# Kernel optimization log

Hardware: AMD Instinct MI355X
Metric: run time of the kernel (lower is better)

Reference implementation:

```python
import jax, jax.numpy as jnp
import numpy as np

D = 384
EPS = 1e-12  # F.normalize eps


def setup_inputs() -> dict:
    key = jax.random.key(0)
    ks = jax.random.split(key, 12)
    s = 1.0 / np.sqrt(D)  # torch Linear default init scale
    return {
        "x": jax.random.normal(ks[0], (8192, D), jnp.float32),
        "y": jax.random.normal(ks[1], (8192, D), jnp.float32),
        "Wq": jax.random.uniform(ks[2], (D, D), jnp.float32, -s, s),
        "bq": jax.random.uniform(ks[3], (D,), jnp.float32, -s, s),
        "Wk": jax.random.uniform(ks[4], (D, D), jnp.float32, -s, s),
        "bk": jax.random.uniform(ks[5], (D,), jnp.float32, -s, s),
        "Wv": jax.random.uniform(ks[6], (D, D), jnp.float32, -s, s),
        "bv": jax.random.uniform(ks[7], (D,), jnp.float32, -s, s),
        "Wo": jax.random.uniform(ks[8], (D, D), jnp.float32, -s, s),
        "bo": jax.random.uniform(ks[9], (D,), jnp.float32, -s, s),
    }


def reference(x, y, Wq, bq, Wk, bk, Wv, bv, Wo, bo):
    # Q: [N, d], K/V: [M, d]
    Q = x @ Wq.T + bq
    K = y @ Wk.T + bk
    V = y @ Wv.T + bv
    scale = 1.0 / jnp.sqrt(jnp.asarray(Q.shape[-1], Q.dtype))
    attn = jax.nn.softmax((Q @ K.T) * scale, axis=-1)  # [N, M]
    ctx = attn @ V  # [N, d]
    # F.normalize(p=2, dim=1): divide by max(||row||_2, eps)
    norm = jnp.maximum(jnp.linalg.norm(ctx, axis=1, keepdims=True), EPS)
    ctx = ctx / norm
    return (x + ctx) @ Wo.T + bo
```

## Files before the change

### kernel.cpp

```cpp
#include <hip/hip_runtime.h>
#include <stdint.h>


typedef __attribute__((ext_vector_type(8))) short bf16x8;
typedef __attribute__((ext_vector_type(4))) float f32x4;
typedef __attribute__((ext_vector_type(16))) float f32x16;

#define DEV static __device__ __forceinline__

DEV short f2bf(float f) {
  uint32_t u = __builtin_bit_cast(uint32_t, f);
  u += 0x7fffu + ((u >> 16) & 1u);
  return (short)(u >> 16);
}
DEV uint32_t pack2(float a, float b) {
  return (uint32_t)(uint16_t)f2bf(a) | ((uint32_t)(uint16_t)f2bf(b) << 16);
}
DEV unsigned cvt_pk(float lo, float hi) {
  unsigned r;
  asm("v_cvt_pk_bf16_f32 %0, %1, %2" : "=v"(r) : "v"(lo), "v"(hi));
  return r;
}
DEV void pl32swap(unsigned& a, unsigned& b) {
  asm volatile("v_permlane32_swap_b32 %0, %1" : "+v"(a), "+v"(b));
}
DEV void gload16(const void* g, void* l) {
  __builtin_amdgcn_global_load_lds(
      (const __attribute__((address_space(1))) unsigned*)g,
      (__attribute__((address_space(3))) unsigned*)l, 16, 0, 0);
}

template <int BIAS_ON_N, int OUT_F32, int A_F32>
__global__ __launch_bounds__(256) void gemm_nt(
    const void* __restrict__ Aptr, const float* __restrict__ B,
    const float* __restrict__ bias, void* __restrict__ Cptr,
    int M, int N, int K, float scale) {
  __shared__ char As[128 * 128];
  __shared__ char Bs[128 * 128];
  const int tid = threadIdx.x;
  const int l = tid & 63, w = tid >> 6;
  const int lq = l & 15, lk = l >> 4;
  const int m0 = blockIdx.x * 128, n0 = blockIdx.y * 128;
  const int wr = (w >> 1) * 64, wc = (w & 1) * 64;
  f32x4 acc[4][4] = {};

  for (int k0 = 0; k0 < K; k0 += 64) {
    if (A_F32) {
      const float* A = (const float*)Aptr;
#pragma unroll
      for (int i = 0; i < 8; i++) {
        int c = tid + i * 256;
        int row = c >> 4, col = (c & 15) * 4;
        f32x4 v = *(const f32x4*)(A + (size_t)(m0 + row) * K + k0 + col);
        uint32_t lo = pack2(v.x, v.y), hi = pack2(v.z, v.w);
        int off = (row * 128 + col * 2) ^ ((row & 7) << 4);
        *(uint32_t*)(As + off) = lo;
        *(uint32_t*)(As + off + 4) = hi;
      }
    } else {
      const short* A = (const short*)Aptr;
#pragma unroll
      for (int i = 0; i < 4; i++) {
        int c = tid + i * 256;
        int row = c >> 3, col = (c & 7) * 8;
        uint4 v = *(const uint4*)(A + (size_t)(m0 + row) * K + k0 + col);
        int off = (row * 128 + col * 2) ^ ((row & 7) << 4);
        *(uint4*)(As + off) = v;
      }
    }
#pragma unroll
    for (int i = 0; i < 8; i++) {
      int c = tid + i * 256;
      int row = c >> 4, col = (c & 15) * 4;
      f32x4 v = *(const f32x4*)(B + (size_t)(n0 + row) * K + k0 + col);
      uint32_t lo = pack2(v.x, v.y), hi = pack2(v.z, v.w);
      int off = (row * 128 + col * 2) ^ ((row & 7) << 4);
      *(uint32_t*)(Bs + off) = lo;
      *(uint32_t*)(Bs + off + 4) = hi;
    }
    __syncthreads();
#pragma unroll
    for (int ks = 0; ks < 2; ks++) {
      bf16x8 af[4], bfr[4];
#pragma unroll
      for (int m = 0; m < 4; m++) {
        int row = wr + m * 16 + lq;
        af[m] = *(const bf16x8*)(As + ((row * 128 + ks * 64 + lk * 16) ^ ((row & 7) << 4)));
      }
#pragma unroll
      for (int n = 0; n < 4; n++) {
        int row = wc + n * 16 + lq;
        bfr[n] = *(const bf16x8*)(Bs + ((row * 128 + ks * 64 + lk * 16) ^ ((row & 7) << 4)));
      }
#pragma unroll
      for (int m = 0; m < 4; m++)
#pragma unroll
        for (int n = 0; n < 4; n++)
          acc[m][n] = __builtin_amdgcn_mfma_f32_16x16x32_bf16(af[m], bfr[n], acc[m][n], 0, 0, 0);
    }
    __syncthreads();
  }
#pragma unroll
  for (int m = 0; m < 4; m++) {
    int mg = m0 + wr + m * 16 + lk * 4;
#pragma unroll
    for (int n = 0; n < 4; n++) {
      int ng = n0 + wc + n * 16 + lq;
#pragma unroll
      for (int r = 0; r < 4; r++) {
        float v = (acc[m][n][r] + (BIAS_ON_N ? bias[ng] : bias[mg + r])) * scale;
        if (OUT_F32)
          ((float*)Cptr)[(size_t)(mg + r) * N + ng] = v;
        else
          ((short*)Cptr)[(size_t)(mg + r) * N + ng] = f2bf(v);
      }
    }
  }
}

#define ITERS 64

__global__ __launch_bounds__(512)
__attribute__((amdgpu_waves_per_eu(2, 2))) void flash_attn(
    const short* __restrict__ Qb, const short* __restrict__ Kb,
    const short* __restrict__ Vt, float* __restrict__ ctx_part) {
  __shared__ char Ks[2][24576];
  __shared__ char Vs[3][24576];
  __shared__ char Ps[2][4][2048];
  const int tid = threadIdx.x, l = tid & 63, w = tid >> 6;
  const int l31 = l & 31, h = l >> 5;
  const int qh = w & 3, dh = w >> 2;
  const int sp = blockIdx.x & 3, qt = blockIdx.x >> 2;
  const int q0 = qt * 128 + qh * 32;
  const int kvbase = sp * 2048;
  const int pswz = ((l31 >> 2) & 7) << 4;
  const int poff = (l31 * 32 + h * 16) ^ pswz;

  int off6[6];
  const int cb = (w & 3) * 6144;
  if (dh == 0) {
#pragma unroll
    for (int i = 0; i < 6; i++) {
      int d = cb + i * 1024 + l * 16;
      int krow = d / 768, kc = d - krow * 768;
      off6[i] = krow * 768 + (kc ^ ((krow & 7) << 4));
    }
  } else {
#pragma unroll
    for (int i = 0; i < 6; i++) {
      int d = cb + i * 1024 + l * 16;
      int vrow = d >> 6, vc = d & 63;
      off6[i] = vrow * 16384 + (vc ^ (((vrow >> 1) & 3) << 4));
    }
  }

  bf16x8 qf[24];
  {
    const short* qrow = Qb + (size_t)(q0 + l31) * 384 + h * 8;
#pragma unroll
    for (int s = 0; s < 24; s++) qf[s] = *(const bf16x8*)(qrow + s * 16);
  }

  if (dh == 0) {
    const char* kb = (const char*)Kb + (size_t)kvbase * 768;
#pragma unroll
    for (int i = 0; i < 6; i++) gload16(kb + off6[i], Ks[0] + cb + i * 1024);
  } else {
    const char* vb = (const char*)Vt + (size_t)kvbase * 2;
#pragma unroll
    for (int i = 0; i < 6; i++) gload16(vb + off6[i], Vs[0] + cb + i * 1024);
  }

  f32x16 acc[6] = {};
  __syncthreads();

#pragma unroll 1
  for (int t = 0; t < ITERS; t++) {
    if (t < ITERS - 1) {
      int kv0 = kvbase + (t + 1) * 32;
      if (dh == 0) {
        const char* kb = (const char*)Kb + (size_t)kv0 * 768;
        char* dst = Ks[(t + 1) & 1] + cb;
#pragma unroll
        for (int i = 0; i < 6; i++) gload16(kb + off6[i], dst + i * 1024);
      } else {
        const char* vb = (const char*)Vt + (size_t)kv0 * 2;
        char* dst = Vs[(t + 1) % 3] + cb;
#pragma unroll
        for (int i = 0; i < 6; i++) gload16(vb + off6[i], dst + i * 1024);
      }
    }

    if (dh == (t & 1)) {
      f32x16 S = {};
      const char* kcb = Ks[t & 1] + l31 * 768;
      const int swzk = (l31 & 7) << 4;
      __builtin_amdgcn_s_setprio(1);
#pragma unroll
      for (int s = 0; s < 24; s++) {
        bf16x8 k0 = *(const bf16x8*)(kcb + ((s * 32 + h * 16) ^ swzk));
        S = __builtin_amdgcn_mfma_f32_32x32x16_bf16(k0, qf[s], S, 0, 0, 0);
      }
      __builtin_amdgcn_s_setprio(0);
      unsigned a0 = cvt_pk(__builtin_amdgcn_exp2f(S[0]), __builtin_amdgcn_exp2f(S[1]));
      unsigned a1 = cvt_pk(__builtin_amdgcn_exp2f(S[2]), __builtin_amdgcn_exp2f(S[3]));
      unsigned a2 = cvt_pk(__builtin_amdgcn_exp2f(S[4]), __builtin_amdgcn_exp2f(S[5]));
      unsigned a3 = cvt_pk(__builtin_amdgcn_exp2f(S[6]), __builtin_amdgcn_exp2f(S[7]));
      pl32swap(a0, a2); pl32swap(a1, a3);
      uint4 pw0 = {a0, a1, a2, a3};
      unsigned b0 = cvt_pk(__builtin_amdgcn_exp2f(S[8]), __builtin_amdgcn_exp2f(S[9]));
      unsigned b1 = cvt_pk(__builtin_amdgcn_exp2f(S[10]), __builtin_amdgcn_exp2f(S[11]));
      unsigned b2 = cvt_pk(__builtin_amdgcn_exp2f(S[12]), __builtin_amdgcn_exp2f(S[13]));
      unsigned b3 = cvt_pk(__builtin_amdgcn_exp2f(S[14]), __builtin_amdgcn_exp2f(S[15]));
      pl32swap(b0, b2); pl32swap(b1, b3);
      uint4 pw1 = {b0, b1, b2, b3};
      char* pwb = Ps[t & 1][qh];
      *(uint4*)(pwb + poff) = pw0;
      *(uint4*)(pwb + 1024 + poff) = pw1;
    }

    if (t > 0) {
      const char* pb = Ps[(t - 1) & 1][qh];
      bf16x8 pf0 = *(const bf16x8*)(pb + poff);
      bf16x8 pf1 = *(const bf16x8*)(pb + 1024 + poff);
      const char* vb = Vs[(t - 1) % 3];
      __builtin_amdgcn_s_setprio(1);
#pragma unroll
      for (int nf = 0; nf < 6; nf++) {
        int vr = dh * 192 + nf * 32 + l31;
        int swz = ((vr >> 1) & 3) << 4;
        const char* vrow = vb + vr * 64;
        bf16x8 v0 = *(const bf16x8*)(vrow + ((h * 16) ^ swz));
        bf16x8 v1 = *(const bf16x8*)(vrow + ((32 + h * 16) ^ swz));
        acc[nf] = __builtin_amdgcn_mfma_f32_32x32x16_bf16(v0, pf0, acc[nf], 0, 0, 0);
        acc[nf] = __builtin_amdgcn_mfma_f32_32x32x16_bf16(v1, pf1, acc[nf], 0, 0, 0);
      }
      __builtin_amdgcn_s_setprio(0);
    }
    __syncthreads();
  }

  {
    const char* pb = Ps[(ITERS - 1) & 1][qh];
    bf16x8 pf0 = *(const bf16x8*)(pb + poff);
    bf16x8 pf1 = *(const bf16x8*)(pb + 1024 + poff);
    const char* vb = Vs[(ITERS - 1) % 3];
#pragma unroll
    for (int nf = 0; nf < 6; nf++) {
      int vr = dh * 192 + nf * 32 + l31;
      int swz = ((vr >> 1) & 3) << 4;
      const char* vrow = vb + vr * 64;
      bf16x8 v0 = *(const bf16x8*)(vrow + ((h * 16) ^ swz));
      bf16x8 v1 = *(const bf16x8*)(vrow + ((32 + h * 16) ^ swz));
      acc[nf] = __builtin_amdgcn_mfma_f32_32x32x16_bf16(v0, pf0, acc[nf], 0, 0, 0);
      acc[nf] = __builtin_amdgcn_mfma_f32_32x32x16_bf16(v1, pf1, acc[nf], 0, 0, 0);
    }
  }

  float* outp = ctx_part + (size_t)sp * 8192 * 384 + (size_t)(q0 + l31) * 384;
#pragma unroll
  for (int nf = 0; nf < 6; nf++) {
#pragma unroll
    for (int qd = 0; qd < 4; qd++) {
      f32x4 v = {acc[nf][qd * 4 + 0], acc[nf][qd * 4 + 1],
                 acc[nf][qd * 4 + 2], acc[nf][qd * 4 + 3]};
      *(f32x4*)(outp + dh * 192 + nf * 32 + qd * 8 + h * 4) = v;
    }
  }
}

__global__ __launch_bounds__(256) void combine_norm(
    const float* __restrict__ ctx_part, const float* __restrict__ x,
    short* __restrict__ Xn) {
  const int l = threadIdx.x & 63, w = threadIdx.x >> 6;
  const int q = blockIdx.x * 4 + w;
  const size_t SLAB = (size_t)8192 * 384;
  float v[6];
  float ss = 0.f;
#pragma unroll
  for (int i = 0; i < 6; i++) {
    size_t off = (size_t)q * 384 + i * 64 + l;
    float s = ctx_part[off] + ctx_part[off + SLAB] + ctx_part[off + 2 * SLAB] +
              ctx_part[off + 3 * SLAB];
    v[i] = s;
    ss += s * s;
  }
#pragma unroll
  for (int m = 1; m <= 32; m <<= 1) ss += __shfl_xor(ss, m);
  float inv = 1.0f / fmaxf(sqrtf(ss), 1e-12f);
#pragma unroll
  for (int i = 0; i < 6; i++) {
    size_t off = (size_t)q * 384 + i * 64 + l;
    Xn[off] = f2bf(x[off] + v[i] * inv);
  }
}

extern "C" void kernel_launch(void* const* d_in, const int* in_sizes, int n_in,
                              void* d_out, int out_size, void* d_ws, size_t ws_size,
                              hipStream_t stream) {
  (void)in_sizes; (void)n_in; (void)out_size; (void)ws_size;
  const float* x  = (const float*)d_in[0];
  const float* y  = (const float*)d_in[1];
  const float* Wq = (const float*)d_in[2];
  const float* bq = (const float*)d_in[3];
  const float* Wk = (const float*)d_in[4];
  const float* bk = (const float*)d_in[5];
  const float* Wv = (const float*)d_in[6];
  const float* bv = (const float*)d_in[7];
  const float* Wo = (const float*)d_in[8];
  const float* bo = (const float*)d_in[9];

  char* ws = (char*)d_ws;
  short* Qb = (short*)(ws);
  short* Kb = (short*)(ws + 6291456);
  short* Vt = (short*)(ws + 12582912);
  short* Xn = (short*)(ws + 18874368);
  float* ctx = (float*)(ws + 25165824);

  const float SC = 0.07362233f;
  dim3 blk(256);
  gemm_nt<1, 0, 1><<<dim3(64, 3), blk, 0, stream>>>(x, Wq, bq, Qb, 8192, 384, 384, SC);
  gemm_nt<1, 0, 1><<<dim3(64, 3), blk, 0, stream>>>(y, Wk, bk, Kb, 8192, 384, 384, 1.0f);
  gemm_nt<0, 0, 1><<<dim3(3, 64), blk, 0, stream>>>(Wv, y, bv, Vt, 384, 8192, 384, 1.0f);
  flash_attn<<<dim3(256), dim3(512), 0, stream>>>(Qb, Kb, Vt, ctx);
  combine_norm<<<dim3(2048), blk, 0, stream>>>(ctx, x, Xn);
  gemm_nt<1, 1, 0><<<dim3(64, 3), blk, 0, stream>>>(Xn, Wo, bo, (float*)d_out, 8192, 384, 384, 1.0f);
}
```

Before: 302.0 us.

## Restructure flash attention prefetch with triple-buffered K and split barriers

K tiles are now triple-buffered and prefetched two iterations ahead, while V drops to double buffering and is issued after a mid-iteration barrier. The single __syncthreads is replaced by explicit vmcnt/lgkmcnt waits and s_barrier calls, so outstanding global loads can stay in flight across the barrier instead of being drained each iteration. The aim is to hide global-to-LDS latency better. The cost is two barriers per iteration and fragile hand-tuned waitcnt values that depend on how many gload16 instructions each wave has issued.

```diff
diff --git a/kernel.cpp b/kernel.cpp
--- a/kernel.cpp
+++ b/kernel.cpp
@@ -124,8 +124,8 @@
 __attribute__((amdgpu_waves_per_eu(2, 2))) void flash_attn(
     const short* __restrict__ Qb, const short* __restrict__ Kb,
     const short* __restrict__ Vt, float* __restrict__ ctx_part) {
-  __shared__ char Ks[2][24576];
-  __shared__ char Vs[3][24576];
+  __shared__ char Ks[3][24576];
+  __shared__ char Vs[2][24576];
   __shared__ char Ps[2][4][2048];
   const int tid = threadIdx.x, l = tid & 63, w = tid >> 6;
   const int l31 = l & 31, h = l >> 5;
@@ -162,38 +162,39 @@
   }
 
   if (dh == 0) {
-    const char* kb = (const char*)Kb + (size_t)kvbase * 768;
-#pragma unroll
-    for (int i = 0; i < 6; i++) gload16(kb + off6[i], Ks[0] + cb + i * 1024);
+    const char* kb0 = (const char*)Kb + (size_t)kvbase * 768;
+#pragma unroll
+    for (int i = 0; i < 6; i++) gload16(kb0 + off6[i], Ks[0] + cb + i * 1024);
+    const char* kb1 = (const char*)Kb + (size_t)(kvbase + 32) * 768;
+#pragma unroll
+    for (int i = 0; i < 6; i++) gload16(kb1 + off6[i], Ks[1] + cb + i * 1024);
   } else {
-    const char* vb = (const char*)Vt + (size_t)kvbase * 2;
-#pragma unroll
-    for (int i = 0; i < 6; i++) gload16(vb + off6[i], Vs[0] + cb + i * 1024);
+    const char* vb0 = (const char*)Vt + (size_t)kvbase * 2;
+#pragma unroll
+    for (int i = 0; i < 6; i++) gload16(vb0 + off6[i], Vs[0] + cb + i * 1024);
   }
 
   f32x16 acc[6] = {};
-  __syncthreads();
 
 #pragma unroll 1
   for (int t = 0; t < ITERS; t++) {
-    if (t < ITERS - 1) {
-      int kv0 = kvbase + (t + 1) * 32;
-      if (dh == 0) {
-        const char* kb = (const char*)Kb + (size_t)kv0 * 768;
-        char* dst = Ks[(t + 1) & 1] + cb;
-#pragma unroll
-        for (int i = 0; i < 6; i++) gload16(kb + off6[i], dst + i * 1024);
-      } else {
-        const char* vb = (const char*)Vt + (size_t)kv0 * 2;
-        char* dst = Vs[(t + 1) % 3] + cb;
-#pragma unroll
-        for (int i = 0; i < 6; i++) gload16(vb + off6[i], dst + i * 1024);
-      }
+    if (t == ITERS - 1)
+      asm volatile("s_waitcnt vmcnt(0)" ::: "memory");
+    else
+      asm volatile("s_waitcnt vmcnt(6)" ::: "memory");
+    asm volatile("s_waitcnt lgkmcnt(0)" ::: "memory");
+    __builtin_amdgcn_s_barrier();
+
+    if (dh == 0 && t + 2 < ITERS) {
+      const char* kb = (const char*)Kb + (size_t)(kvbase + (t + 2) * 32) * 768;
+      char* dst = Ks[(t + 2) % 3] + cb;
+#pragma unroll
+      for (int i = 0; i < 6; i++) gload16(kb + off6[i], dst + i * 1024);
     }
 
     if (dh == (t & 1)) {
       f32x16 S = {};
-      const char* kcb = Ks[t & 1] + l31 * 768;
+      const char* kcb = Ks[t % 3] + l31 * 768;
       const int swzk = (l31 & 7) << 4;
       __builtin_amdgcn_s_setprio(1);
 #pragma unroll
@@ -223,7 +224,7 @@
       const char* pb = Ps[(t - 1) & 1][qh];
       bf16x8 pf0 = *(const bf16x8*)(pb + poff);
       bf16x8 pf1 = *(const bf16x8*)(pb + 1024 + poff);
-      const char* vb = Vs[(t - 1) % 3];
+      const char* vb = Vs[(t - 1) & 1];
       __builtin_amdgcn_s_setprio(1);
 #pragma unroll
       for (int nf = 0; nf < 6; nf++) {
@@ -237,14 +238,25 @@
       }
       __builtin_amdgcn_s_setprio(0);
     }
-    __syncthreads();
-  }
-
+
+    asm volatile("s_waitcnt lgkmcnt(0)" ::: "memory");
+    __builtin_amdgcn_s_barrier();
+    if (dh == 1 && t + 1 < ITERS) {
+      const char* vb = (const char*)Vt + (size_t)(kvbase + (t + 1) * 32) * 2;
+      char* dst = Vs[(t + 1) & 1] + cb;
+#pragma unroll
+      for (int i = 0; i < 6; i++) gload16(vb + off6[i], dst + i * 1024);
+    }
+  }
+
+  asm volatile("s_waitcnt vmcnt(0)" ::: "memory");
+  asm volatile("s_waitcnt lgkmcnt(0)" ::: "memory");
+  __builtin_amdgcn_s_barrier();
   {
     const char* pb = Ps[(ITERS - 1) & 1][qh];
     bf16x8 pf0 = *(const bf16x8*)(pb + poff);
     bf16x8 pf1 = *(const bf16x8*)(pb + 1024 + poff);
-    const char* vb = Vs[(ITERS - 1) % 3];
+    const char* vb = Vs[(ITERS - 1) & 1];
 #pragma unroll
     for (int nf = 0; nf < 6; nf++) {
       int vr = dh * 192 + nf * 32 + l31;
@@ -323,6 +335,6 @@
   gemm_nt<1, 0, 1><<<dim3(64, 3), blk, 0, stream>>>(y, Wk, bk, Kb, 8192, 384, 384, 1.0f);
   gemm_nt<0, 0, 1><<<dim3(3, 64), blk, 0, stream>>>(Wv, y, bv, Vt, 384, 8192, 384, 1.0f);
   flash_attn<<<dim3(256), dim3(512), 0, stream>>>(Qb, Kb, Vt, ctx);
-  combine_norm<<<dim3(2048), blk, 0, stream>>>(ctx, x, Xn);
+  combine_norm<<<dim3(2048), dim3(256), 0, stream>>>(ctx, x, Xn);
   gemm_nt<1, 1, 0><<<dim3(64, 3), blk, 0, stream>>>(Xn, Wo, bo, (float*)d_out, 8192, 384, 384, 1.0f);
 }
```

Result: slower. 346.1 us (+14.6%).
